# Optimization experiments

Hardware: AMD Instinct MI355X
Metric: run time of the kernel (lower is better)

The kernel has to match this reference:

```python
import jax, jax.numpy as jnp
import numpy as np


def setup_inputs() -> dict:
    key = jax.random.key(0)
    k1, k2 = jax.random.split(key)
    flow = jax.random.normal(k1, (4, 2, 256, 256), dtype=jnp.float32)   # [B,2,H,W] per-pixel flow over dt
    spike = jax.random.uniform(k2, (4, 64, 256, 256), dtype=jnp.float32)  # [B,C,H,W] spike voxel grid
    return {"flow": flow, "spike": spike}


def _splat(vals, xn, yn, H, W):
    """Forward bilinear splat of vals [H,W] to continuous coords (xn,yn) [H,W]."""
    x0 = jnp.floor(xn)
    y0 = jnp.floor(yn)
    wx = xn - x0  # fractional weights (differentiable w.r.t. flow)
    wy = yn - y0
    x0i = x0.astype(jnp.int32)
    y0i = y0.astype(jnp.int32)
    out = jnp.zeros(H * W, dtype=vals.dtype)
    corners = (
        (0, 0, (1.0 - wx) * (1.0 - wy)),
        (1, 0, wx * (1.0 - wy)),
        (0, 1, (1.0 - wx) * wy),
        (1, 1, wx * wy),
    )
    for dx, dy, w in corners:
        xi = x0i + dx
        yi = y0i + dy
        valid = (xi >= 0) & (xi < W) & (yi >= 0) & (yi < H)
        idx = jnp.clip(yi, 0, H - 1) * W + jnp.clip(xi, 0, W - 1)
        out = out.at[idx.ravel()].add(jnp.where(valid, w * vals, 0.0).ravel())
    return out.reshape(H, W)


def spike_warp_mid(spike, flow, dt):
    """Warp each time bin c by flow * (c - mid)/dt toward the middle timestamp (bilinear splat)."""
    B, C, H, W = spike.shape
    mid = (C - 1) / 2.0
    yy, xx = jnp.meshgrid(jnp.arange(H, dtype=spike.dtype),
                          jnp.arange(W, dtype=spike.dtype), indexing='ij')
    s = (jnp.arange(C, dtype=spike.dtype) - mid) / jnp.asarray(dt, spike.dtype)  # [C]
    u = flow[:, 0][:, None]  # [B,1,H,W]
    v = flow[:, 1][:, None]
    xn = xx + u * s[None, :, None, None]  # [B,C,H,W]
    yn = yy + v * s[None, :, None, None]
    splat_bc = jax.vmap(jax.vmap(lambda va, xa, ya: _splat(va, xa, ya, H, W)))
    return splat_bc(spike, xn, yn)  # [B,C,H,W]


def reference(flow, spike):
    B, C, H, W = spike.shape
    spike_warped = spike_warp_mid(spike, flow, dt=64)
    # Faithful to original: sum over BATCH dim inside per-batch loop (same each iter),
    # so loss = (B * -var) / B = -var(spike_image) with unbiased variance.
    spike_image = jnp.sum(spike_warped, axis=0)  # [C,H,W]
    loss = -jnp.var(spike_image - jnp.mean(spike_image), ddof=1)
    return loss
```

## Files before the change

kernel.cpp:

```cpp
#include <hip/hip_runtime.h>

typedef float f2 __attribute__((ext_vector_type(2)));

constexpr int B = 4, C = 64, H = 256, W = 256;
constexpr int HW = H * W;
constexpr long long N_TOT = (long long)C * HW;

constexpr int TS = 16;
constexpr int R = 4;
constexpr int SW = 24;
constexpr int PS = 25;
constexpr int SAREA = SW * SW;
constexpr int NBLK = 256 * 8;

template <int RX>
__device__ __forceinline__ void row_gather(
    const f2* __restrict__ uvrow, const f2* __restrict__ sprow,
    f2 sm0, f2 sm1, f2 sm2, f2 sm3, f2 fdy2,
    f2& a0, f2& a1, f2& a2, f2& a3) {
#pragma unroll
  for (int dx = -RX; dx <= RX; ++dx) {
    f2 u2 = uvrow[dx];
    const f2* vp = sprow + dx * 4;
    const f2 fdx2 = (float)dx;
    const f2 ux = f2{u2.x, u2.x};
    const f2 vy = f2{u2.y, u2.y};
    f2 ay0 = __builtin_elementwise_fma(vy, sm0, fdy2);
    f2 ay1 = __builtin_elementwise_fma(vy, sm1, fdy2);
    f2 ay2 = __builtin_elementwise_fma(vy, sm2, fdy2);
    f2 ay3 = __builtin_elementwise_fma(vy, sm3, fdy2);
    f2 ax0 = __builtin_elementwise_fma(ux, sm0, fdx2);
    f2 ax1 = __builtin_elementwise_fma(ux, sm1, fdx2);
    f2 ax2 = __builtin_elementwise_fma(ux, sm2, fdx2);
    f2 ax3 = __builtin_elementwise_fma(ux, sm3, fdx2);
    const f2 z = f2{0.f, 0.f};
    f2 tx0 = __builtin_elementwise_max(1.0f - __builtin_elementwise_abs(ax0), z);
    f2 ty0 = __builtin_elementwise_max(1.0f - __builtin_elementwise_abs(ay0), z);
    f2 tx1 = __builtin_elementwise_max(1.0f - __builtin_elementwise_abs(ax1), z);
    f2 ty1 = __builtin_elementwise_max(1.0f - __builtin_elementwise_abs(ay1), z);
    f2 tx2 = __builtin_elementwise_max(1.0f - __builtin_elementwise_abs(ax2), z);
    f2 ty2 = __builtin_elementwise_max(1.0f - __builtin_elementwise_abs(ay2), z);
    f2 tx3 = __builtin_elementwise_max(1.0f - __builtin_elementwise_abs(ax3), z);
    f2 ty3 = __builtin_elementwise_max(1.0f - __builtin_elementwise_abs(ay3), z);
    a0 = __builtin_elementwise_fma(tx0 * ty0, vp[0], a0);
    a1 = __builtin_elementwise_fma(tx1 * ty1, vp[1], a1);
    a2 = __builtin_elementwise_fma(tx2 * ty2, vp[2], a2);
    a3 = __builtin_elementwise_fma(tx3 * ty3, vp[3], a3);
  }
}

__global__ __launch_bounds__(256) void fused_kernel(
    const float* __restrict__ flow,
    const float* __restrict__ spike,
    double* __restrict__ partials) {
  __shared__ f2 uv[SW * PS];
  __shared__ f2 spk[SW * PS * 4];
  __shared__ float wmx[4], wmy[4];
  __shared__ double red[8];

  const int bid = blockIdx.x;
  const int tile = bid & 255;
  const int j = bid >> 8;
  const int tx0 = (tile & 15) * TS;
  const int ty0 = (tile >> 4) * TS;
  const int tid = threadIdx.x;
  const int qx = tid & 15, qy = tid >> 4;
  const int wave = tid >> 6;

  f2 smv[4];
  float smag3;
#pragma unroll
  for (int t = 0; t < 4; ++t) {
    float sm = ((float)(4 * j + t) + 0.5f) * (1.0f / 64.0f);
    smv[t] = f2{-sm, sm};
    if (t == 3) smag3 = sm;
  }
  const int cn0 = 31 - 4 * j;
  const int cp0 = 32 + 4 * j;

  f2 a0 = {0.f, 0.f}, a1 = {0.f, 0.f}, a2 = {0.f, 0.f}, a3 = {0.f, 0.f};

  bool c_act[3], c_val[3];
  int c_apos[3], c_gp[3];
#pragma unroll
  for (int k = 0; k < 3; ++k) {
    int pos = tid + 256 * k;
    c_act[k] = pos < SAREA;
    int row = pos / SW;
    int col = pos - row * SW;
    c_apos[k] = row * PS + col;
    int gy = ty0 + row - R, gx = tx0 + col - R;
    c_val[k] = c_act[k] & ((unsigned)gy < (unsigned)H) & ((unsigned)gx < (unsigned)W);
    c_gp[k] = gy * W + gx;
  }

  float p_u[3], p_v[3];
  float4 p_a[3], p_b[3];

  auto prefetch = [&](int b) {
    const float* fu = flow + (size_t)b * 2 * HW;
    const float* fv = fu + HW;
    const float* spb = spike + (size_t)b * C * HW;
#pragma unroll
    for (int k = 0; k < 3; ++k) {
      float u = 0.f, v = 0.f;
      float4 a = {0.f, 0.f, 0.f, 0.f};
      float4 d = {0.f, 0.f, 0.f, 0.f};
      if (c_val[k]) {
        int gp = c_gp[k];
        u = fu[gp];
        v = fv[gp];
        a.x = spb[(size_t)cn0 * HW + gp];
        a.y = spb[(size_t)(cn0 - 1) * HW + gp];
        a.z = spb[(size_t)(cn0 - 2) * HW + gp];
        a.w = spb[(size_t)(cn0 - 3) * HW + gp];
        d.x = spb[(size_t)cp0 * HW + gp];
        d.y = spb[(size_t)(cp0 + 1) * HW + gp];
        d.z = spb[(size_t)(cp0 + 2) * HW + gp];
        d.w = spb[(size_t)(cp0 + 3) * HW + gp];
      }
      p_u[k] = u; p_v[k] = v; p_a[k] = a; p_b[k] = d;
    }
  };

  prefetch(0);

  const int qpos = (qy + R) * PS + (qx + R);

  for (int b = 0; b < B; ++b) {
    float mu = 0.f, mv = 0.f;
#pragma unroll
    for (int k = 0; k < 3; ++k) {
      if (c_act[k]) {
        int ap = c_apos[k];
        uv[ap] = f2{p_u[k], p_v[k]};
        f2* sp = &spk[ap * 4];
        sp[0] = f2{p_a[k].x, p_b[k].x};
        sp[1] = f2{p_a[k].y, p_b[k].y};
        sp[2] = f2{p_a[k].z, p_b[k].z};
        sp[3] = f2{p_a[k].w, p_b[k].w};
        mu = fmaxf(mu, fabsf(p_u[k]));
        mv = fmaxf(mv, fabsf(p_v[k]));
      }
    }
    for (int off = 32; off > 0; off >>= 1) {
      mu = fmaxf(mu, __shfl_down(mu, off, 64));
      mv = fmaxf(mv, __shfl_down(mv, off, 64));
    }
    if ((tid & 63) == 0) { wmx[wave] = mu; wmy[wave] = mv; }
    __syncthreads();
    float bu = fmaxf(fmaxf(wmx[0], wmx[1]), fmaxf(wmx[2], wmx[3]));
    float bv = fmaxf(fmaxf(wmy[0], wmy[1]), fmaxf(wmy[2], wmy[3]));
    int rx = min((int)(1.0f + bu * smag3), R);
    int ry = min((int)(1.0f + bv * smag3), R);

    if (b + 1 < B) prefetch(b + 1);

    for (int dy = -ry; dy <= ry; ++dy) {
      const int rp = qpos + dy * PS;
      const f2* uvrow = &uv[rp];
      const f2* sprow = &spk[rp * 4];
      const f2 fdy2 = (float)dy;
      if (rx == 1)
        row_gather<1>(uvrow, sprow, smv[0], smv[1], smv[2], smv[3], fdy2, a0, a1, a2, a3);
      else if (rx == 2)
        row_gather<2>(uvrow, sprow, smv[0], smv[1], smv[2], smv[3], fdy2, a0, a1, a2, a3);
      else if (rx == 3)
        row_gather<3>(uvrow, sprow, smv[0], smv[1], smv[2], smv[3], fdy2, a0, a1, a2, a3);
      else
        row_gather<4>(uvrow, sprow, smv[0], smv[1], smv[2], smv[3], fdy2, a0, a1, a2, a3);
    }
    __syncthreads();
  }

  double ls = 0.0, lq = 0.0;
  {
    double x;
    x = (double)a0.x; ls += x; lq += x * x;
    x = (double)a0.y; ls += x; lq += x * x;
    x = (double)a1.x; ls += x; lq += x * x;
    x = (double)a1.y; ls += x; lq += x * x;
    x = (double)a2.x; ls += x; lq += x * x;
    x = (double)a2.y; ls += x; lq += x * x;
    x = (double)a3.x; ls += x; lq += x * x;
    x = (double)a3.y; ls += x; lq += x * x;
  }
  for (int off = 32; off > 0; off >>= 1) {
    ls += __shfl_down(ls, off, 64);
    lq += __shfl_down(lq, off, 64);
  }
  if ((tid & 63) == 0) { red[wave * 2] = ls; red[wave * 2 + 1] = lq; }
  __syncthreads();
  if (tid == 0) {
    partials[2 * bid] = red[0] + red[2] + red[4] + red[6];
    partials[2 * bid + 1] = red[1] + red[3] + red[5] + red[7];
  }
}

__global__ __launch_bounds__(256) void finalize_kernel(
    const double* __restrict__ partials, float* __restrict__ out) {
  double s = 0.0, q = 0.0;
  for (int i = threadIdx.x; i < NBLK; i += 256) {
    s += partials[2 * i];
    q += partials[2 * i + 1];
  }
  for (int off = 32; off > 0; off >>= 1) {
    s += __shfl_down(s, off, 64);
    q += __shfl_down(q, off, 64);
  }
  __shared__ double ss[4], qq[4];
  int lane = threadIdx.x & 63;
  int wave = threadIdx.x >> 6;
  if (lane == 0) { ss[wave] = s; qq[wave] = q; }
  __syncthreads();
  if (threadIdx.x == 0) {
    double sum = ss[0] + ss[1] + ss[2] + ss[3];
    double sq = qq[0] + qq[1] + qq[2] + qq[3];
    double n = (double)N_TOT;
    double var = (sq - sum * sum / n) / (n - 1.0);
    out[0] = (float)(-var);
  }
}

extern "C" void kernel_launch(void* const* d_in, const int* in_sizes, int n_in,
                              void* d_out, int out_size, void* d_ws, size_t ws_size,
                              hipStream_t stream) {
  const float* flow = (const float*)d_in[0];
  const float* spike = (const float*)d_in[1];
  float* out = (float*)d_out;
  double* partials = (double*)d_ws;

  fused_kernel<<<dim3(NBLK), dim3(256), 0, stream>>>(flow, spike, partials);
  finalize_kernel<<<1, dim3(256), 0, stream>>>(partials, out);
}
```

Before: 164.7 us.

## Halve channels per block, doubling grid, and use runtime dx loop

Each block now handles 2 mirrored channel pairs instead of 4, so the grid doubles to 4096 blocks and the shared-memory spike tile halves. The templated per-radius row_gather dispatch is replaced by a plain runtime dx loop. The intent is more parallelism and occupancy, with less LDS and fewer registers per block. In exchange every block redundantly reloads the flow halo and repeats the max-flow reduction, and the runtime loop may not unroll as well as the templates did.

After: 166.3 us. About the same (+1.0%).

```diff
diff --git a/kernel.cpp b/kernel.cpp
--- a/kernel.cpp
+++ b/kernel.cpp
@@ -11,50 +11,15 @@
 constexpr int SW = 24;
 constexpr int PS = 25;
 constexpr int SAREA = SW * SW;
-constexpr int NBLK = 256 * 8;
-
-template <int RX>
-__device__ __forceinline__ void row_gather(
-    const f2* __restrict__ uvrow, const f2* __restrict__ sprow,
-    f2 sm0, f2 sm1, f2 sm2, f2 sm3, f2 fdy2,
-    f2& a0, f2& a1, f2& a2, f2& a3) {
-#pragma unroll
-  for (int dx = -RX; dx <= RX; ++dx) {
-    f2 u2 = uvrow[dx];
-    const f2* vp = sprow + dx * 4;
-    const f2 fdx2 = (float)dx;
-    const f2 ux = f2{u2.x, u2.x};
-    const f2 vy = f2{u2.y, u2.y};
-    f2 ay0 = __builtin_elementwise_fma(vy, sm0, fdy2);
-    f2 ay1 = __builtin_elementwise_fma(vy, sm1, fdy2);
-    f2 ay2 = __builtin_elementwise_fma(vy, sm2, fdy2);
-    f2 ay3 = __builtin_elementwise_fma(vy, sm3, fdy2);
-    f2 ax0 = __builtin_elementwise_fma(ux, sm0, fdx2);
-    f2 ax1 = __builtin_elementwise_fma(ux, sm1, fdx2);
-    f2 ax2 = __builtin_elementwise_fma(ux, sm2, fdx2);
-    f2 ax3 = __builtin_elementwise_fma(ux, sm3, fdx2);
-    const f2 z = f2{0.f, 0.f};
-    f2 tx0 = __builtin_elementwise_max(1.0f - __builtin_elementwise_abs(ax0), z);
-    f2 ty0 = __builtin_elementwise_max(1.0f - __builtin_elementwise_abs(ay0), z);
-    f2 tx1 = __builtin_elementwise_max(1.0f - __builtin_elementwise_abs(ax1), z);
-    f2 ty1 = __builtin_elementwise_max(1.0f - __builtin_elementwise_abs(ay1), z);
-    f2 tx2 = __builtin_elementwise_max(1.0f - __builtin_elementwise_abs(ax2), z);
-    f2 ty2 = __builtin_elementwise_max(1.0f - __builtin_elementwise_abs(ay2), z);
-    f2 tx3 = __builtin_elementwise_max(1.0f - __builtin_elementwise_abs(ax3), z);
-    f2 ty3 = __builtin_elementwise_max(1.0f - __builtin_elementwise_abs(ay3), z);
-    a0 = __builtin_elementwise_fma(tx0 * ty0, vp[0], a0);
-    a1 = __builtin_elementwise_fma(tx1 * ty1, vp[1], a1);
-    a2 = __builtin_elementwise_fma(tx2 * ty2, vp[2], a2);
-    a3 = __builtin_elementwise_fma(tx3 * ty3, vp[3], a3);
-  }
-}
+constexpr int NCHUNK = 16;
+constexpr int NBLK = 256 * NCHUNK;
 
 __global__ __launch_bounds__(256) void fused_kernel(
     const float* __restrict__ flow,
     const float* __restrict__ spike,
     double* __restrict__ partials) {
   __shared__ f2 uv[SW * PS];
-  __shared__ f2 spk[SW * PS * 4];
+  __shared__ f2 spk[SW * PS * 2];
   __shared__ float wmx[4], wmy[4];
   __shared__ double red[8];
 
@@ -67,18 +32,14 @@
   const int qx = tid & 15, qy = tid >> 4;
   const int wave = tid >> 6;
 
-  f2 smv[4];
-  float smag3;
-#pragma unroll
-  for (int t = 0; t < 4; ++t) {
-    float sm = ((float)(4 * j + t) + 0.5f) * (1.0f / 64.0f);
-    smv[t] = f2{-sm, sm};
-    if (t == 3) smag3 = sm;
-  }
-  const int cn0 = 31 - 4 * j;
-  const int cp0 = 32 + 4 * j;
+  const float s0 = ((float)(2 * j) + 0.5f) * (1.0f / 64.0f);
+  const float s1 = ((float)(2 * j + 1) + 0.5f) * (1.0f / 64.0f);
+  const f2 sm0 = f2{-s0, s0};
+  const f2 sm1 = f2{-s1, s1};
+  const int cn0 = 31 - 2 * j;
+  const int cp0 = 32 + 2 * j;
 
-  f2 a0 = {0.f, 0.f}, a1 = {0.f, 0.f}, a2 = {0.f, 0.f}, a3 = {0.f, 0.f};
+  f2 a0 = {0.f, 0.f}, a1 = {0.f, 0.f};
 
   bool c_act[3], c_val[3];
   int c_apos[3], c_gp[3];
@@ -95,7 +56,7 @@
   }
 
   float p_u[3], p_v[3];
-  float4 p_a[3], p_b[3];
+  f2 p_a[3], p_b[3];
 
   auto prefetch = [&](int b) {
     const float* fu = flow + (size_t)b * 2 * HW;
@@ -104,20 +65,15 @@
 #pragma unroll
     for (int k = 0; k < 3; ++k) {
       float u = 0.f, v = 0.f;
-      float4 a = {0.f, 0.f, 0.f, 0.f};
-      float4 d = {0.f, 0.f, 0.f, 0.f};
+      f2 a = {0.f, 0.f}, d = {0.f, 0.f};
       if (c_val[k]) {
         int gp = c_gp[k];
         u = fu[gp];
         v = fv[gp];
         a.x = spb[(size_t)cn0 * HW + gp];
-        a.y = spb[(size_t)(cn0 - 1) * HW + gp];
-        a.z = spb[(size_t)(cn0 - 2) * HW + gp];
-        a.w = spb[(size_t)(cn0 - 3) * HW + gp];
-        d.x = spb[(size_t)cp0 * HW + gp];
+        a.y = spb[(size_t)cp0 * HW + gp];
+        d.x = spb[(size_t)(cn0 - 1) * HW + gp];
         d.y = spb[(size_t)(cp0 + 1) * HW + gp];
-        d.z = spb[(size_t)(cp0 + 2) * HW + gp];
-        d.w = spb[(size_t)(cp0 + 3) * HW + gp];
       }
       p_u[k] = u; p_v[k] = v; p_a[k] = a; p_b[k] = d;
     }
@@ -134,11 +90,9 @@
       if (c_act[k]) {
         int ap = c_apos[k];
         uv[ap] = f2{p_u[k], p_v[k]};
-        f2* sp = &spk[ap * 4];
-        sp[0] = f2{p_a[k].x, p_b[k].x};
-        sp[1] = f2{p_a[k].y, p_b[k].y};
-        sp[2] = f2{p_a[k].z, p_b[k].z};
-        sp[3] = f2{p_a[k].w, p_b[k].w};
+        f2* sp = &spk[ap * 2];
+        sp[0] = p_a[k];
+        sp[1] = p_b[k];
         mu = fmaxf(mu, fabsf(p_u[k]));
         mv = fmaxf(mv, fabsf(p_v[k]));
       }
@@ -151,24 +105,33 @@
     __syncthreads();
     float bu = fmaxf(fmaxf(wmx[0], wmx[1]), fmaxf(wmx[2], wmx[3]));
     float bv = fmaxf(fmaxf(wmy[0], wmy[1]), fmaxf(wmy[2], wmy[3]));
-    int rx = min((int)(1.0f + bu * smag3), R);
-    int ry = min((int)(1.0f + bv * smag3), R);
+    int rx = min((int)(1.0f + bu * s1), R);
+    int ry = min((int)(1.0f + bv * s1), R);
 
     if (b + 1 < B) prefetch(b + 1);
 
     for (int dy = -ry; dy <= ry; ++dy) {
+      const f2 fdy2 = (float)dy;
       const int rp = qpos + dy * PS;
-      const f2* uvrow = &uv[rp];
-      const f2* sprow = &spk[rp * 4];
-      const f2 fdy2 = (float)dy;
-      if (rx == 1)
-        row_gather<1>(uvrow, sprow, smv[0], smv[1], smv[2], smv[3], fdy2, a0, a1, a2, a3);
-      else if (rx == 2)
-        row_gather<2>(uvrow, sprow, smv[0], smv[1], smv[2], smv[3], fdy2, a0, a1, a2, a3);
-      else if (rx == 3)
-        row_gather<3>(uvrow, sprow, smv[0], smv[1], smv[2], smv[3], fdy2, a0, a1, a2, a3);
-      else
-        row_gather<4>(uvrow, sprow, smv[0], smv[1], smv[2], smv[3], fdy2, a0, a1, a2, a3);
+      for (int dx = -rx; dx <= rx; ++dx) {
+        const int pp = rp + dx;
+        f2 u2 = uv[pp];
+        const f2* vp = &spk[pp * 2];
+        const f2 fdx2 = (float)dx;
+        const f2 ux = f2{u2.x, u2.x};
+        const f2 vy = f2{u2.y, u2.y};
+        const f2 z = f2{0.f, 0.f};
+        f2 ax0 = __builtin_elementwise_fma(ux, sm0, fdx2);
+        f2 ay0 = __builtin_elementwise_fma(vy, sm0, fdy2);
+        f2 ax1 = __builtin_elementwise_fma(ux, sm1, fdx2);
+        f2 ay1 = __builtin_elementwise_fma(vy, sm1, fdy2);
+        f2 tx0 = __builtin_elementwise_max(1.0f - __builtin_elementwise_abs(ax0), z);
+        f2 ty0 = __builtin_elementwise_max(1.0f - __builtin_elementwise_abs(ay0), z);
+        f2 tx1 = __builtin_elementwise_max(1.0f - __builtin_elementwise_abs(ax1), z);
+        f2 ty1 = __builtin_elementwise_max(1.0f - __builtin_elementwise_abs(ay1), z);
+        a0 = __builtin_elementwise_fma(tx0 * ty0, vp[0], a0);
+        a1 = __builtin_elementwise_fma(tx1 * ty1, vp[1], a1);
+      }
     }
     __syncthreads();
   }
@@ -180,10 +143,6 @@
     x = (double)a0.y; ls += x; lq += x * x;
     x = (double)a1.x; ls += x; lq += x * x;
     x = (double)a1.y; ls += x; lq += x * x;
-    x = (double)a2.x; ls += x; lq += x * x;
-    x = (double)a2.y; ls += x; lq += x * x;
-    x = (double)a3.x; ls += x; lq += x * x;
-    x = (double)a3.y; ls += x; lq += x * x;
   }
   for (int off = 32; off > 0; off >>= 1) {
     ls += __shfl_down(ls, off, 64);
```
